# Performance work log

Measured on AMD Instinct MI355X. Metric: run time of the kernel, lower is better.

The kernel has to match this reference:

```python
import jax, jax.numpy as jnp
import numpy as np

# Module constants derived from init_kwargs
T = 8           # number of tables / features
ROWS = 100000   # rows per table
D = 128         # embedding dim (uniform across tables)
B = 8192        # batch size (bags per feature)
L = 32          # avg bag length
N = T * B * L   # total indices


def setup_inputs() -> dict:
    key = jax.random.key(0)
    k_idx, k_w = jax.random.split(key)
    indices = jax.random.randint(k_idx, (N,), 0, ROWS, dtype=jnp.int64)
    # CSR offsets: T*B+1 bag boundaries, uniform bag length L
    offsets = (jnp.arange(T * B + 1, dtype=jnp.int64) * L)
    # Concatenated embedding tables: [T*ROWS, D] (fbgemm init ~ U(-0.01, 0.01))
    weights = jax.random.uniform(k_w, (T * ROWS, D), dtype=jnp.float32,
                                 minval=-0.01, maxval=0.01)
    return {"indices": indices, "offsets": offsets, "weights": weights}


def reference(indices, offsets, weights):
    # hash_size_cumsum: start row of each table in the concatenated weights
    hash_size_cumsum = jnp.arange(T, dtype=indices.dtype) * ROWS
    # segment id (bag id) for each index element from CSR offsets
    seg = jnp.searchsorted(offsets, jnp.arange(indices.shape[0]), side='right') - 1
    # which table each bag belongs to (bags laid out table-major: T x B)
    table_id = seg // B
    global_idx = indices + hash_size_cumsum[table_id]
    emb = weights[global_idx]                                   # [N, D] gather
    pooled = jax.ops.segment_sum(emb, seg, num_segments=T * B)  # [T*B, D] sum pool
    # [T, B, D] -> [B, T, D] -> [B, total_D]  (feature-concatenated output)
    return pooled.reshape(T, B, D).transpose(1, 0, 2).reshape(B, T * D)
```

## Files before the change

kernel.cpp:

```cpp
#include <hip/hip_runtime.h>

constexpr int T    = 8;
constexpr int ROWS = 100000;
constexpr int D    = 128;
constexpr int B    = 8192;
constexpr int BAGS = T * B;
constexpr int GROUPS_PER_BLOCK = 8;

__global__ __launch_bounds__(256) void emb_bag_pool_kernel(
    const int*   __restrict__ indices,
    const int*   __restrict__ offsets,
    const float* __restrict__ weights,
    float*       __restrict__ out)
{
    const int lane = threadIdx.x & 31;
    const int seg  = blockIdx.x * GROUPS_PER_BLOCK + (threadIdx.x >> 5);
    if (seg >= BAGS) return;

    const int t = seg >> 13;
    const int b = seg & (B - 1);

    const int start = offsets[seg];
    const int end   = offsets[seg + 1];

    const size_t table_base = (size_t)t * (size_t)ROWS;

    float4 acc0 = make_float4(0.f, 0.f, 0.f, 0.f);
    float4 acc1 = make_float4(0.f, 0.f, 0.f, 0.f);

    for (int base = start; base < end; base += 32) {
        const int chunk = min(32, end - base);
        int my_idx = (lane < chunk) ? indices[base + lane] : 0;

        if (chunk == 32) {
            #pragma unroll
            for (int r = 0; r < 32; r += 2) {
                const int row0 = __shfl(my_idx, r,     32);
                const int row1 = __shfl(my_idx, r + 1, 32);
                const float4* w0 = (const float4*)(weights + (table_base + (size_t)row0) * D);
                const float4* w1 = (const float4*)(weights + (table_base + (size_t)row1) * D);
                const float4 v0 = w0[lane];
                const float4 v1 = w1[lane];
                acc0.x += v0.x; acc0.y += v0.y; acc0.z += v0.z; acc0.w += v0.w;
                acc1.x += v1.x; acc1.y += v1.y; acc1.z += v1.z; acc1.w += v1.w;
            }
        } else {
            for (int r = 0; r < chunk; ++r) {
                const int row = __shfl(my_idx, r, 32);
                const float4* w = (const float4*)(weights + (table_base + (size_t)row) * D);
                const float4 v = w[lane];
                acc0.x += v.x; acc0.y += v.y; acc0.z += v.z; acc0.w += v.w;
            }
        }
    }

    const float4 acc = make_float4(acc0.x + acc1.x, acc0.y + acc1.y,
                                   acc0.z + acc1.z, acc0.w + acc1.w);

    float4* orow = (float4*)(out + (size_t)b * (size_t)(T * D) + (size_t)t * D);
    orow[lane] = acc;
}

extern "C" void kernel_launch(void* const* d_in, const int* in_sizes, int n_in,
                              void* d_out, int out_size, void* d_ws, size_t ws_size,
                              hipStream_t stream) {
    const int*   indices = (const int*)d_in[0];
    const int*   offsets = (const int*)d_in[1];
    const float* weights = (const float*)d_in[2];
    float*       out     = (float*)d_out;

    const int grid = BAGS / GROUPS_PER_BLOCK;
    emb_bag_pool_kernel<<<grid, 256, 0, stream>>>(indices, offsets, weights, out);
}
```

Baseline: 565.0 us.

## Map one bag per 64-lane wavefront with float2 loads and scalar row indices

```diff
diff --git a/kernel.cpp b/kernel.cpp
--- a/kernel.cpp
+++ b/kernel.cpp
@@ -5,7 +5,9 @@
 constexpr int D    = 128;
 constexpr int B    = 8192;
 constexpr int BAGS = T * B;
-constexpr int GROUPS_PER_BLOCK = 8;
+constexpr int WAVES_PER_BLOCK = 4;
+
+typedef float v2f __attribute__((ext_vector_type(2)));
 
 __global__ __launch_bounds__(256) void emb_bag_pool_kernel(
     const int*   __restrict__ indices,
@@ -13,52 +15,42 @@
     const float* __restrict__ weights,
     float*       __restrict__ out)
 {
-    const int lane = threadIdx.x & 31;
-    const int seg  = blockIdx.x * GROUPS_PER_BLOCK + (threadIdx.x >> 5);
+    const int lane = threadIdx.x & 63;
+    const int seg  = blockIdx.x * WAVES_PER_BLOCK + (threadIdx.x >> 6);
     if (seg >= BAGS) return;
 
     const int t = seg >> 13;
     const int b = seg & (B - 1);
 
-    const int start = offsets[seg];
-    const int end   = offsets[seg + 1];
+    const int start = __builtin_amdgcn_readfirstlane(offsets[seg]);
+    const int end   = __builtin_amdgcn_readfirstlane(offsets[seg + 1]);
+    const int len   = end - start;
 
-    const size_t table_base = (size_t)t * (size_t)ROWS;
+    const float* tbase = weights + (size_t)t * (size_t)ROWS * (size_t)D;
 
-    float4 acc0 = make_float4(0.f, 0.f, 0.f, 0.f);
-    float4 acc1 = make_float4(0.f, 0.f, 0.f, 0.f);
+    v2f acc = {0.f, 0.f};
 
-    for (int base = start; base < end; base += 32) {
-        const int chunk = min(32, end - base);
-        int my_idx = (lane < chunk) ? indices[base + lane] : 0;
+    if (len == 32) {
+        const int vidx = (lane < 32) ? indices[start + lane] : 0;
 
-        if (chunk == 32) {
-            #pragma unroll
-            for (int r = 0; r < 32; r += 2) {
-                const int row0 = __shfl(my_idx, r,     32);
-                const int row1 = __shfl(my_idx, r + 1, 32);
-                const float4* w0 = (const float4*)(weights + (table_base + (size_t)row0) * D);
-                const float4* w1 = (const float4*)(weights + (table_base + (size_t)row1) * D);
-                const float4 v0 = w0[lane];
-                const float4 v1 = w1[lane];
-                acc0.x += v0.x; acc0.y += v0.y; acc0.z += v0.z; acc0.w += v0.w;
-                acc1.x += v1.x; acc1.y += v1.y; acc1.z += v1.z; acc1.w += v1.w;
-            }
-        } else {
-            for (int r = 0; r < chunk; ++r) {
-                const int row = __shfl(my_idx, r, 32);
-                const float4* w = (const float4*)(weights + (table_base + (size_t)row) * D);
-                const float4 v = w[lane];
-                acc0.x += v.x; acc0.y += v.y; acc0.z += v.z; acc0.w += v.w;
-            }
+        #pragma unroll
+        for (int r = 0; r < 32; ++r) {
+            const int row = __builtin_amdgcn_readlane(vidx, r);
+            const v2f* wr = (const v2f*)(tbase + (size_t)row * D);
+            const v2f v = wr[lane];
+            acc += v;
+        }
+    } else {
+        for (int r = 0; r < len; ++r) {
+            const int row = __builtin_amdgcn_readfirstlane(indices[start + r]);
+            const v2f* wr = (const v2f*)(tbase + (size_t)row * D);
+            const v2f v = wr[lane];
+            acc += v;
         }
     }
 
-    const float4 acc = make_float4(acc0.x + acc1.x, acc0.y + acc1.y,
-                                   acc0.z + acc1.z, acc0.w + acc1.w);
-
-    float4* orow = (float4*)(out + (size_t)b * (size_t)(T * D) + (size_t)t * D);
-    orow[lane] = acc;
+    v2f* orow = (v2f*)(out + (size_t)b * (size_t)(T * D) + (size_t)t * D);
+    __builtin_nontemporal_store(acc, orow + lane);
 }
 
 extern "C" void kernel_launch(void* const* d_in, const int* in_sizes, int n_in,
@@ -69,6 +61,6 @@
     const float* weights = (const float*)d_in[2];
     float*       out     = (float*)d_out;
 
-    const int grid = BAGS / GROUPS_PER_BLOCK;
+    const int grid = BAGS / WAVES_PER_BLOCK;
     emb_bag_pool_kernel<<<grid, 256, 0, stream>>>(indices, offsets, weights, out);
 }
```

New measurement: 597.1 us. 5.7% more time.
